# Performance work log

Measured on AMD Instinct MI355X. Metric: run time of the kernel, lower is better.

## Reference

```python
import jax, jax.numpy as jnp
import numpy as np

N_NODES = 50000


def _gcn_norm(edge_index, num_nodes):
    # Add self-loops (PyG GCNConv default) and compute symmetric norm.
    loops = jnp.arange(num_nodes, dtype=edge_index.dtype)
    src = jnp.concatenate([edge_index[0], loops])
    dst = jnp.concatenate([edge_index[1], loops])
    ones = jnp.ones(src.shape[0], dtype=jnp.float32)
    deg = jax.ops.segment_sum(ones, dst, num_segments=num_nodes)
    deg_inv_sqrt = jnp.where(deg > 0, jax.lax.rsqrt(jnp.maximum(deg, 1.0)), 0.0)
    norm = deg_inv_sqrt[src] * deg_inv_sqrt[dst]  # [E + N]
    return src, dst, norm


def _gcn_conv(x, src, dst, norm, W, b, num_nodes):
    xw = x @ W                               # [N, out]
    msg = xw[src] * norm[:, None]            # gather + scale  [E+N, out]
    out = jax.ops.segment_sum(msg, dst, num_segments=num_nodes)  # scatter-add
    return out + b


def setup_inputs() -> dict:
    key = jax.random.key(0)
    ks = jax.random.split(key, 10)
    d_in, d_h, d_out = 64, 64, 8
    n_edges = 800000
    x = jax.random.normal(ks[0], (N_NODES, d_in), dtype=jnp.float32)
    edge_index = jax.random.randint(ks[1], (2, n_edges), 0, N_NODES, dtype=jnp.int64)
    def w(k, fan_in, fan_out):
        return jax.random.normal(k, (fan_in, fan_out), dtype=jnp.float32) * (1.0 / np.sqrt(fan_in))
    return {
        "x": x,
        "edge_index": edge_index,
        "W0": w(ks[2], d_in, d_h), "b0": jnp.zeros((d_h,), jnp.float32),
        "W1": w(ks[3], d_h, d_h), "b1": jnp.zeros((d_h,), jnp.float32),
        "W2": w(ks[4], d_h, d_h), "b2": jnp.zeros((d_h,), jnp.float32),
        "linW": w(ks[5], d_h, d_out), "linb": jnp.zeros((d_out,), jnp.float32),
    }


def reference(x, edge_index, W0, b0, W1, b1, W2, b2, linW, linb):
    num_nodes = x.shape[0]
    src, dst, norm = _gcn_norm(edge_index, num_nodes)
    # 3 GCNConv layers, ReLU; dropout is identity at inference (training=False).
    for W, b in ((W0, b0), (W1, b1), (W2, b2)):
        x = jax.nn.relu(_gcn_conv(x, src, dst, norm, W, b, num_nodes))
    return x @ linW + linb
```

## Files before the change

kernel.cpp:

```cpp
#include <hip/hip_runtime.h>
#include <hip/hip_fp16.h>

#define TPB 256
#define CAP 16384
#define CAPSH 14
#define SC_BLOCKS 256
#define MAXE 16


__device__ __forceinline__ int ld_idx(const void* p, long long i, int is64) {
    return is64 ? (int)((const long long*)p)[i] : ((const int*)p)[i];
}

__device__ __forceinline__ float4 h4_to_f4(ushort4 v) {
    float4 r;
    r.x = __half2float(__ushort_as_half(v.x));
    r.y = __half2float(__ushort_as_half(v.y));
    r.z = __half2float(__ushort_as_half(v.z));
    r.w = __half2float(__ushort_as_half(v.w));
    return r;
}

__device__ __forceinline__ ushort4 f4_to_h4(float4 v) {
    ushort4 r;
    r.x = __half_as_ushort(__float2half_rn(v.x));
    r.y = __half_as_ushort(__float2half_rn(v.y));
    r.z = __half_as_ushort(__float2half_rn(v.z));
    r.w = __half_as_ushort(__float2half_rn(v.w));
    return r;
}

__global__ __launch_bounds__(TPB) void p3_scatter(const void* ei, long long E,
                                                  int* gcur, int* pairs) {
    __shared__ int cnt[TPB];
    __shared__ int cur2[TPB];
    __shared__ int s_is64;
    int t = threadIdx.x;
    if (t < 64) {
        const unsigned int* w = (const unsigned int*)ei;
        unsigned long long m = __ballot(w[2 * t + 1] != 0u);
        if (t == 0) s_is64 = (m == 0ull) ? 1 : 0;
    }
    cnt[t] = 0;
    __syncthreads();
    const int is64 = s_is64;
    long long chunk = (E + SC_BLOCKS - 1) / SC_BLOCKS;
    long long s0 = (long long)blockIdx.x * chunk;
    long long s1 = (s0 + chunk < E) ? s0 + chunk : E;

    int pk[MAXE];
    int bk[MAXE];
    int ne = 0;
    #pragma unroll
    for (int i = 0; i < MAXE; ++i) {
        long long e = s0 + t + (long long)i * TPB;
        if (e < s1) {
            int sv = ld_idx(ei, e, is64);
            int d  = ld_idx(ei, E + e, is64);
            pk[i] = (sv << 8) | (d & 255);
            bk[i] = d >> 8;
            atomicAdd(&cnt[bk[i]], 1);
            ne++;
        }
    }
    __syncthreads();
    if (cnt[t]) cur2[t] = (t << CAPSH) + atomicAdd(&gcur[t], cnt[t]);
    __syncthreads();
    #pragma unroll
    for (int i = 0; i < MAXE; ++i) {
        if (i < ne) {
            int pos = atomicAdd(&cur2[bk[i]], 1);
            pairs[pos] = pk[i];
        }
    }
}

__global__ __launch_bounds__(TPB) void p4_fill(const int* __restrict__ pairs,
                                               const int* __restrict__ gcur,
                                               const float* __restrict__ x,
                                               int2* __restrict__ meta,
                                               int* __restrict__ csr,
                                               ushort4* __restrict__ z0, int N) {
    __shared__ int ldeg[TPB];
    __shared__ int ssc[TPB];
    __shared__ int cur[TPB];
    __shared__ float fdis[TPB];
    int t = threadIdx.x;
    int b = blockIdx.x;
    int base = b << CAPSH;
    int ecnt = gcur[b];
    ldeg[t] = 0;
    __syncthreads();
    for (int e = base + t; e < base + ecnt; e += TPB)
        atomicAdd(&ldeg[pairs[e] & 255], 1);
    __syncthreads();
    int dv = ldeg[t];
    int pv = (dv + 15) & ~15;
    ssc[t] = pv;
    __syncthreads();
    for (int off = 1; off < TPB; off <<= 1) {
        int u = 0;
        if (t >= off) u = ssc[t - off];
        __syncthreads();
        ssc[t] += u;
        __syncthreads();
    }
    int o = base + ssc[t] - pv;
    cur[t] = o;
    float dd = rsqrtf((float)(dv + 1));
    fdis[t] = dd;
    int node = (b << 8) + t;
    if (node < N)
        meta[node] = make_int2((o << 7) | (pv >> 4), __float_as_int(dd));
    __syncthreads();
    for (int e = base + t; e < base + ecnt; e += TPB) {
        int p = pairs[e];
        int pos = atomicAdd(&cur[p & 255], 1);
        csr[pos] = p >> 8;
    }
    for (int e = o + dv; e < o + pv; ++e) csr[e] = N;

    int ni = t >> 4, c = t & 15;
    for (int p = 0; p < 16; ++p) {
        int nd = (b << 8) + p * 16 + ni;
        if (nd < N) {
            float dvv = fdis[p * 16 + ni];
            float4 h = ((const float4*)x)[(size_t)nd * 16 + c];
            float4 r = {h.x * dvv, h.y * dvv, h.z * dvv, h.w * dvv};
            z0[(size_t)nd * 16 + c] = f4_to_h4(r);
        }
    }
    if (b == 0 && t < 16) z0[(size_t)N * 16 + t] = make_ushort4(0, 0, 0, 0);
}

__device__ __forceinline__ float4 gather_rows(const ushort4* __restrict__ y4,
                                              const int* __restrict__ csr,
                                              int start, int nbatch, int c,
                                              float4 acc) {
    const int base = threadIdx.x & 48;
    int idx = (nbatch > 0) ? csr[start + c] : 0;
    for (int bt = 0; bt < nbatch; ++bt) {
        int nidx = (bt + 1 < nbatch) ? csr[start + (bt + 1) * 16 + c] : 0;
        #pragma unroll
        for (int k = 0; k < 16; ++k) {
            int s = __shfl(idx, base + k);
            float4 v = h4_to_f4(y4[(size_t)s * 16 + c]);
            acc.x += v.x; acc.y += v.y; acc.z += v.z; acc.w += v.w;
        }
        idx = nidx;
    }
    return acc;
}

__device__ __forceinline__ float4 shfl_mm(float4 s, const float4* Ws4, int c) {
    const int base = threadIdx.x & 48;
    float4 u = {0.f, 0.f, 0.f, 0.f};
    #pragma unroll
    for (int r = 0; r < 4; ++r) {
        float sr = (r == 0) ? s.x : (r == 1) ? s.y : (r == 2) ? s.z : s.w;
        #pragma unroll
        for (int q = 0; q < 16; ++q) {
            float hv = __shfl(sr, base + q);
            float4 w = Ws4[(q * 4 + r) * 16 + c];
            u.x = fmaf(hv, w.x, u.x);
            u.y = fmaf(hv, w.y, u.y);
            u.z = fmaf(hv, w.z, u.z);
            u.w = fmaf(hv, w.w, u.w);
        }
    }
    return u;
}

__global__ __launch_bounds__(TPB) void layer_mm(const ushort4* __restrict__ z,
                                                const int* __restrict__ csr,
                                                const int2* __restrict__ meta,
                                                const float* __restrict__ b,
                                                const float* __restrict__ W,
                                                ushort4* __restrict__ zout, int n) {
    __shared__ float Ws[64 * 64];
    int t = threadIdx.x;
    float4* Ws4 = (float4*)Ws;
    const float4* W4g = (const float4*)W;
    #pragma unroll
    for (int i = 0; i < 4; ++i) Ws4[t + i * TPB] = W4g[t + i * TPB];

    if (blockIdx.x == 0 && t < 16)
        zout[(size_t)n * 16 + t] = make_ushort4(0, 0, 0, 0);

    int ni = t >> 4, c = t & 15;
    int node = blockIdx.x * 16 + ni;
    float4 s = {0.f, 0.f, 0.f, 0.f};
    float dv = 0.f;
    if (node < n) {
        int2 m = meta[node];
        int start = ((unsigned)m.x) >> 7;
        int nbatch = m.x & 127;
        dv = __int_as_float(m.y);
        s = h4_to_f4(z[(size_t)node * 16 + c]);
        s = gather_rows(z, csr, start, nbatch, c, s);
    }
    __syncthreads();
    float4 u = shfl_mm(s, Ws4, c);
    if (node < n) {
        float4 bb = ((const float4*)b)[c];
        float4 r;
        r.x = fmaxf(fmaf(dv, u.x, bb.x), 0.f) * dv;
        r.y = fmaxf(fmaf(dv, u.y, bb.y), 0.f) * dv;
        r.z = fmaxf(fmaf(dv, u.z, bb.z), 0.f) * dv;
        r.w = fmaxf(fmaf(dv, u.w, bb.w), 0.f) * dv;
        zout[(size_t)node * 16 + c] = f4_to_h4(r);
    }
}

__global__ __launch_bounds__(TPB) void layer_final(const ushort4* __restrict__ z,
                                                   const int* __restrict__ csr,
                                                   const int2* __restrict__ meta,
                                                   const float* __restrict__ b,
                                                   const float* __restrict__ W,
                                                   const float* __restrict__ Wl,
                                                   const float* __restrict__ bl,
                                                   float* __restrict__ out, int n) {
    __shared__ float Ws[64 * 64];
    __shared__ float Wls[64 * 8];
    __shared__ float bls[8];
    int t = threadIdx.x;
    float4* Ws4 = (float4*)Ws;
    const float4* W4g = (const float4*)W;
    #pragma unroll
    for (int i = 0; i < 4; ++i) Ws4[t + i * TPB] = W4g[t + i * TPB];
    if (t < 128) ((float4*)Wls)[t] = ((const float4*)Wl)[t];
    if (t < 8) bls[t] = bl[t];

    int ni = t >> 4, c = t & 15;
    int node = blockIdx.x * 16 + ni;
    float4 s = {0.f, 0.f, 0.f, 0.f};
    float dv = 0.f;
    if (node < n) {
        int2 m = meta[node];
        int start = ((unsigned)m.x) >> 7;
        int nbatch = m.x & 127;
        dv = __int_as_float(m.y);
        s = h4_to_f4(z[(size_t)node * 16 + c]);
        s = gather_rows(z, csr, start, nbatch, c, s);
    }
    __syncthreads();
    float4 u = shfl_mm(s, Ws4, c);
    float4 bb = ((const float4*)b)[c];
    float4 h;
    h.x = fmaxf(fmaf(dv, u.x, bb.x), 0.f);
    h.y = fmaxf(fmaf(dv, u.y, bb.y), 0.f);
    h.z = fmaxf(fmaf(dv, u.z, bb.z), 0.f);
    h.w = fmaxf(fmaf(dv, u.w, bb.w), 0.f);

    const int base = threadIdx.x & 48;
    int col = c & 7;
    float acc = bls[col];
    #pragma unroll
    for (int r = 0; r < 4; ++r) {
        float hr = (r == 0) ? h.x : (r == 1) ? h.y : (r == 2) ? h.z : h.w;
        #pragma unroll
        for (int q = 0; q < 16; ++q) {
            float hv = __shfl(hr, base + q);
            acc = fmaf(hv, Wls[(q * 4 + r) * 8 + col], acc);
        }
    }
    if (c < 8 && node < n) out[(size_t)node * 8 + col] = acc;
}

extern "C" void kernel_launch(void* const* d_in, const int* in_sizes, int n_in,
                              void* d_out, int out_size, void* d_ws, size_t ws_size,
                              hipStream_t stream) {
    const float* x  = (const float*)d_in[0];
    const void*  ei = d_in[1];
    const float* W0 = (const float*)d_in[2];
    const float* b0 = (const float*)d_in[3];
    const float* W1 = (const float*)d_in[4];
    const float* b1 = (const float*)d_in[5];
    const float* W2 = (const float*)d_in[6];
    const float* b2 = (const float*)d_in[7];
    const float* Wl = (const float*)d_in[8];
    const float* bl = (const float*)d_in[9];

    const long long E = in_sizes[1] / 2;
    const int dh = in_sizes[3];
    const int din = in_sizes[2] / dh;
    const int N = in_sizes[0] / din;
    const int nb = (N + 255) >> 8;

    char* ws = (char*)d_ws;
    size_t off = 0;
    auto alloc = [&](size_t bytes) -> char* {
        char* r = ws + off;
        off += (bytes + 255) & ~(size_t)255;
        return r;
    };
    int*     gcur    = (int*)    alloc(1024);
    int2*    meta    = (int2*)   alloc((size_t)N * 8);
    int*     pairs   = (int*)    alloc((size_t)nb * CAP * 4);
    int*     csr     = (int*)    alloc((size_t)nb * CAP * 4);
    ushort4* zbA     = (ushort4*)alloc((size_t)(N + 1) * 64 * 2);
    ushort4* zbB     = (ushort4*)alloc((size_t)(N + 1) * 64 * 2);

    hipMemsetAsync(gcur, 0, 256 * sizeof(int), stream);
    p3_scatter<<<SC_BLOCKS, TPB, 0, stream>>>(ei, E, gcur, pairs);
    p4_fill<<<nb, TPB, 0, stream>>>(pairs, gcur, x, meta, csr, zbA, N);

    const int gL = (N + 15) / 16;
    layer_mm<<<gL, TPB, 0, stream>>>(zbA, csr, meta, b0, W0, zbB, N);
    layer_mm<<<gL, TPB, 0, stream>>>(zbB, csr, meta, b1, W1, zbA, N);
    layer_final<<<gL, TPB, 0, stream>>>(zbA, csr, meta, b2, W2, Wl, bl,
                                        (float*)d_out, N);
}
```

Baseline: 208.3 us.

## Use 8 lanes per node with 16-byte fp16 loads in layer kernels

Each node row is now handled by 8 lanes, each loading 8 half values (16 bytes), instead of 16 lanes loading 4 halves. Each 256-thread block therefore covers 32 nodes instead of 16. CSR padding per node drops from multiples of 16 to multiples of 8, so fewer padding entries pointing at the zero row are gathered, and the meta packing is changed to match. The aim is to widen gather loads and cut wasted padded gathers. In exchange each lane holds more registers, and each lane does twice the FMAs per shuffle in the small matmul.

```diff
diff --git a/kernel.cpp b/kernel.cpp
--- a/kernel.cpp
+++ b/kernel.cpp
@@ -7,18 +7,12 @@
 #define SC_BLOCKS 256
 #define MAXE 16
 
+typedef __attribute__((ext_vector_type(8))) float f32x8;
+typedef __attribute__((ext_vector_type(8))) unsigned short u16x8;
+
 
 __device__ __forceinline__ int ld_idx(const void* p, long long i, int is64) {
     return is64 ? (int)((const long long*)p)[i] : ((const int*)p)[i];
-}
-
-__device__ __forceinline__ float4 h4_to_f4(ushort4 v) {
-    float4 r;
-    r.x = __half2float(__ushort_as_half(v.x));
-    r.y = __half2float(__ushort_as_half(v.y));
-    r.z = __half2float(__ushort_as_half(v.z));
-    r.w = __half2float(__ushort_as_half(v.w));
-    return r;
 }
 
 __device__ __forceinline__ ushort4 f4_to_h4(float4 v) {
@@ -95,7 +89,7 @@
         atomicAdd(&ldeg[pairs[e] & 255], 1);
     __syncthreads();
     int dv = ldeg[t];
-    int pv = (dv + 15) & ~15;
+    int pv = (dv + 7) & ~7;
     ssc[t] = pv;
     __syncthreads();
     for (int off = 1; off < TPB; off <<= 1) {
@@ -111,7 +105,7 @@
     fdis[t] = dd;
     int node = (b << 8) + t;
     if (node < N)
-        meta[node] = make_int2((o << 7) | (pv >> 4), __float_as_int(dd));
+        meta[node] = make_int2((o << 8) | (pv >> 3), __float_as_int(dd));
     __syncthreads();
     for (int e = base + t; e < base + ecnt; e += TPB) {
         int p = pairs[e];
@@ -133,50 +127,64 @@
     if (b == 0 && t < 16) z0[(size_t)N * 16 + t] = make_ushort4(0, 0, 0, 0);
 }
 
-__device__ __forceinline__ float4 gather_rows(const ushort4* __restrict__ y4,
-                                              const int* __restrict__ csr,
-                                              int start, int nbatch, int c,
-                                              float4 acc) {
-    const int base = threadIdx.x & 48;
+__device__ __forceinline__ f32x8 gather_rows(const u16x8* __restrict__ z8,
+                                             const int* __restrict__ csr,
+                                             int start, int nbatch, int c,
+                                             f32x8 acc) {
+    const int base = threadIdx.x & 56;
     int idx = (nbatch > 0) ? csr[start + c] : 0;
     for (int bt = 0; bt < nbatch; ++bt) {
-        int nidx = (bt + 1 < nbatch) ? csr[start + (bt + 1) * 16 + c] : 0;
-        #pragma unroll
-        for (int k = 0; k < 16; ++k) {
+        int nidx = (bt + 1 < nbatch) ? csr[start + (bt + 1) * 8 + c] : 0;
+        #pragma unroll
+        for (int k = 0; k < 8; ++k) {
             int s = __shfl(idx, base + k);
-            float4 v = h4_to_f4(y4[(size_t)s * 16 + c]);
-            acc.x += v.x; acc.y += v.y; acc.z += v.z; acc.w += v.w;
+            u16x8 v = z8[(size_t)s * 8 + c];
+            #pragma unroll
+            for (int i = 0; i < 8; ++i)
+                acc[i] += __half2float(__ushort_as_half(v[i]));
         }
         idx = nidx;
     }
     return acc;
 }
 
-__device__ __forceinline__ float4 shfl_mm(float4 s, const float4* Ws4, int c) {
-    const int base = threadIdx.x & 48;
-    float4 u = {0.f, 0.f, 0.f, 0.f};
-    #pragma unroll
-    for (int r = 0; r < 4; ++r) {
-        float sr = (r == 0) ? s.x : (r == 1) ? s.y : (r == 2) ? s.z : s.w;
-        #pragma unroll
-        for (int q = 0; q < 16; ++q) {
-            float hv = __shfl(sr, base + q);
-            float4 w = Ws4[(q * 4 + r) * 16 + c];
-            u.x = fmaf(hv, w.x, u.x);
-            u.y = fmaf(hv, w.y, u.y);
-            u.z = fmaf(hv, w.z, u.z);
-            u.w = fmaf(hv, w.w, u.w);
+__device__ __forceinline__ f32x8 shfl_mm8(f32x8 s, const float4* Ws4, int c) {
+    const int base = threadIdx.x & 56;
+    f32x8 u = {0.f, 0.f, 0.f, 0.f, 0.f, 0.f, 0.f, 0.f};
+    #pragma unroll
+    for (int q = 0; q < 8; ++q) {
+        #pragma unroll
+        for (int r = 0; r < 8; ++r) {
+            float hv = __shfl(s[r], base + q);
+            float4 w0 = Ws4[(q * 8 + r) * 16 + 2 * c];
+            float4 w1 = Ws4[(q * 8 + r) * 16 + 2 * c + 1];
+            u[0] = fmaf(hv, w0.x, u[0]);
+            u[1] = fmaf(hv, w0.y, u[1]);
+            u[2] = fmaf(hv, w0.z, u[2]);
+            u[3] = fmaf(hv, w0.w, u[3]);
+            u[4] = fmaf(hv, w1.x, u[4]);
+            u[5] = fmaf(hv, w1.y, u[5]);
+            u[6] = fmaf(hv, w1.z, u[6]);
+            u[7] = fmaf(hv, w1.w, u[7]);
         }
     }
     return u;
 }
 
-__global__ __launch_bounds__(TPB) void layer_mm(const ushort4* __restrict__ z,
+__device__ __forceinline__ u16x8 f8_to_h8(f32x8 v) {
+    u16x8 r;
+    #pragma unroll
+    for (int i = 0; i < 8; ++i)
+        r[i] = __half_as_ushort(__float2half_rn(v[i]));
+    return r;
+}
+
+__global__ __launch_bounds__(TPB) void layer_mm(const u16x8* __restrict__ z,
                                                 const int* __restrict__ csr,
                                                 const int2* __restrict__ meta,
                                                 const float* __restrict__ b,
                                                 const float* __restrict__ W,
-                                                ushort4* __restrict__ zout, int n) {
+                                                u16x8* __restrict__ zout, int n) {
     __shared__ float Ws[64 * 64];
     int t = threadIdx.x;
     float4* Ws4 = (float4*)Ws;
@@ -184,35 +192,45 @@
     #pragma unroll
     for (int i = 0; i < 4; ++i) Ws4[t + i * TPB] = W4g[t + i * TPB];
 
-    if (blockIdx.x == 0 && t < 16)
-        zout[(size_t)n * 16 + t] = make_ushort4(0, 0, 0, 0);
-
-    int ni = t >> 4, c = t & 15;
-    int node = blockIdx.x * 16 + ni;
-    float4 s = {0.f, 0.f, 0.f, 0.f};
+    if (blockIdx.x == 0 && t < 8) {
+        u16x8 zz = {0, 0, 0, 0, 0, 0, 0, 0};
+        zout[(size_t)n * 8 + t] = zz;
+    }
+
+    int wave = t >> 6, lane = t & 63;
+    int g = lane >> 3, c = lane & 7;
+    int node = blockIdx.x * 32 + wave * 8 + g;
+    f32x8 s = {0.f, 0.f, 0.f, 0.f, 0.f, 0.f, 0.f, 0.f};
     float dv = 0.f;
     if (node < n) {
         int2 m = meta[node];
-        int start = ((unsigned)m.x) >> 7;
-        int nbatch = m.x & 127;
+        int start = ((unsigned)m.x) >> 8;
+        int nbatch = m.x & 255;
         dv = __int_as_float(m.y);
-        s = h4_to_f4(z[(size_t)node * 16 + c]);
+        u16x8 v = z[(size_t)node * 8 + c];
+        #pragma unroll
+        for (int i = 0; i < 8; ++i) s[i] = __half2float(__ushort_as_half(v[i]));
         s = gather_rows(z, csr, start, nbatch, c, s);
     }
     __syncthreads();
-    float4 u = shfl_mm(s, Ws4, c);
+    f32x8 u = shfl_mm8(s, Ws4, c);
     if (node < n) {
-        float4 bb = ((const float4*)b)[c];
-        float4 r;
-        r.x = fmaxf(fmaf(dv, u.x, bb.x), 0.f) * dv;
-        r.y = fmaxf(fmaf(dv, u.y, bb.y), 0.f) * dv;
-        r.z = fmaxf(fmaf(dv, u.z, bb.z), 0.f) * dv;
-        r.w = fmaxf(fmaf(dv, u.w, bb.w), 0.f) * dv;
-        zout[(size_t)node * 16 + c] = f4_to_h4(r);
-    }
-}
-
-__global__ __launch_bounds__(TPB) void layer_final(const ushort4* __restrict__ z,
+        float4 b0 = ((const float4*)b)[2 * c];
+        float4 b1 = ((const float4*)b)[2 * c + 1];
+        f32x8 r;
+        r[0] = fmaxf(fmaf(dv, u[0], b0.x), 0.f) * dv;
+        r[1] = fmaxf(fmaf(dv, u[1], b0.y), 0.f) * dv;
+        r[2] = fmaxf(fmaf(dv, u[2], b0.z), 0.f) * dv;
+        r[3] = fmaxf(fmaf(dv, u[3], b0.w), 0.f) * dv;
+        r[4] = fmaxf(fmaf(dv, u[4], b1.x), 0.f) * dv;
+        r[5] = fmaxf(fmaf(dv, u[5], b1.y), 0.f) * dv;
+        r[6] = fmaxf(fmaf(dv, u[6], b1.z), 0.f) * dv;
+        r[7] = fmaxf(fmaf(dv, u[7], b1.w), 0.f) * dv;
+        zout[(size_t)node * 8 + c] = f8_to_h8(r);
+    }
+}
+
+__global__ __launch_bounds__(TPB) void layer_final(const u16x8* __restrict__ z,
                                                    const int* __restrict__ csr,
                                                    const int2* __restrict__ meta,
                                                    const float* __restrict__ b,
@@ -231,40 +249,46 @@
     if (t < 128) ((float4*)Wls)[t] = ((const float4*)Wl)[t];
     if (t < 8) bls[t] = bl[t];
 
-    int ni = t >> 4, c = t & 15;
-    int node = blockIdx.x * 16 + ni;
-    float4 s = {0.f, 0.f, 0.f, 0.f};
+    int wave = t >> 6, lane = t & 63;
+    int g = lane >> 3, c = lane & 7;
+    int node = blockIdx.x * 32 + wave * 8 + g;
+    f32x8 s = {0.f, 0.f, 0.f, 0.f, 0.f, 0.f, 0.f, 0.f};
     float dv = 0.f;
     if (node < n) {
         int2 m = meta[node];
-        int start = ((unsigned)m.x) >> 7;
-        int nbatch = m.x & 127;
+        int start = ((unsigned)m.x) >> 8;
+        int nbatch = m.x & 255;
         dv = __int_as_float(m.y);
-        s = h4_to_f4(z[(size_t)node * 16 + c]);
+        u16x8 v = z[(size_t)node * 8 + c];
+        #pragma unroll
+        for (int i = 0; i < 8; ++i) s[i] = __half2float(__ushort_as_half(v[i]));
         s = gather_rows(z, csr, start, nbatch, c, s);
     }
     __syncthreads();
-    float4 u = shfl_mm(s, Ws4, c);
-    float4 bb = ((const float4*)b)[c];
-    float4 h;
-    h.x = fmaxf(fmaf(dv, u.x, bb.x), 0.f);
-    h.y = fmaxf(fmaf(dv, u.y, bb.y), 0.f);
-    h.z = fmaxf(fmaf(dv, u.z, bb.z), 0.f);
-    h.w = fmaxf(fmaf(dv, u.w, bb.w), 0.f);
-
-    const int base = threadIdx.x & 48;
-    int col = c & 7;
-    float acc = bls[col];
-    #pragma unroll
-    for (int r = 0; r < 4; ++r) {
-        float hr = (r == 0) ? h.x : (r == 1) ? h.y : (r == 2) ? h.z : h.w;
-        #pragma unroll
-        for (int q = 0; q < 16; ++q) {
-            float hv = __shfl(hr, base + q);
-            acc = fmaf(hv, Wls[(q * 4 + r) * 8 + col], acc);
-        }
-    }
-    if (c < 8 && node < n) out[(size_t)node * 8 + col] = acc;
+    f32x8 u = shfl_mm8(s, Ws4, c);
+    float4 b0 = ((const float4*)b)[2 * c];
+    float4 b1 = ((const float4*)b)[2 * c + 1];
+    f32x8 h;
+    h[0] = fmaxf(fmaf(dv, u[0], b0.x), 0.f);
+    h[1] = fmaxf(fmaf(dv, u[1], b0.y), 0.f);
+    h[2] = fmaxf(fmaf(dv, u[2], b0.z), 0.f);
+    h[3] = fmaxf(fmaf(dv, u[3], b0.w), 0.f);
+    h[4] = fmaxf(fmaf(dv, u[4], b1.x), 0.f);
+    h[5] = fmaxf(fmaf(dv, u[5], b1.y), 0.f);
+    h[6] = fmaxf(fmaf(dv, u[6], b1.z), 0.f);
+    h[7] = fmaxf(fmaf(dv, u[7], b1.w), 0.f);
+
+    const int base = threadIdx.x & 56;
+    float acc = bls[c];
+    #pragma unroll
+    for (int q = 0; q < 8; ++q) {
+        #pragma unroll
+        for (int r = 0; r < 8; ++r) {
+            float hv = __shfl(h[r], base + q);
+            acc = fmaf(hv, Wls[(q * 8 + r) * 8 + c], acc);
+        }
+    }
+    if (node < n) out[(size_t)node * 8 + c] = acc;
 }
 
 extern "C" void kernel_launch(void* const* d_in, const int* in_sizes, int n_in,
@@ -294,18 +318,19 @@
         off += (bytes + 255) & ~(size_t)255;
         return r;
     };
-    int*     gcur    = (int*)    alloc(1024);
-    int2*    meta    = (int2*)   alloc((size_t)N * 8);
-    int*     pairs   = (int*)    alloc((size_t)nb * CAP * 4);
-    int*     csr     = (int*)    alloc((size_t)nb * CAP * 4);
-    ushort4* zbA     = (ushort4*)alloc((size_t)(N + 1) * 64 * 2);
-    ushort4* zbB     = (ushort4*)alloc((size_t)(N + 1) * 64 * 2);
+    int*   gcur    = (int*)  alloc(1024);
+    int2*  meta    = (int2*) alloc((size_t)N * 8);
+    int*   pairs   = (int*)  alloc((size_t)nb * CAP * 4);
+    int*   csr     = (int*)  alloc((size_t)nb * CAP * 4);
+    u16x8* zbA     = (u16x8*)alloc((size_t)(N + 1) * 64 * 2);
+    u16x8* zbB     = (u16x8*)alloc((size_t)(N + 1) * 64 * 2);
 
     hipMemsetAsync(gcur, 0, 256 * sizeof(int), stream);
     p3_scatter<<<SC_BLOCKS, TPB, 0, stream>>>(ei, E, gcur, pairs);
-    p4_fill<<<nb, TPB, 0, stream>>>(pairs, gcur, x, meta, csr, zbA, N);
-
-    const int gL = (N + 15) / 16;
+    p4_fill<<<nb, TPB, 0, stream>>>(pairs, gcur, x, meta, csr,
+                                    (ushort4*)zbA, N);
+
+    const int gL = (N + 31) / 32;
     layer_mm<<<gL, TPB, 0, stream>>>(zbA, csr, meta, b0, W0, zbB, N);
     layer_mm<<<gL, TPB, 0, stream>>>(zbB, csr, meta, b1, W1, zbA, N);
     layer_final<<<gL, TPB, 0, stream>>>(zbA, csr, meta, b2, W2, Wl, bl,
```

After: 186.7 us (median of 2 runs). -10.4%, faster.
